# Performance work log

Hardware: AMD Instinct MI355X
Metric: run time of the kernel (lower is better)

Reference implementation:

```python
import jax, jax.numpy as jnp
import numpy as np

DIM = 256
HID = int(DIM * 2.66)        # 680
CH = 2 * HID                 # 1360, TVConv channels
K = 3
K2 = K * K
HP, WP = 14, 14
POSI = 4
INTER = min(64, HID // 2)    # 64
EPS = 1e-5


def conv2d(x, w, pad):
    # x: (B, Cin, H, W), w: (Cout, Cin, kh, kw)
    return jax.lax.conv_general_dilated(
        x, w, window_strides=(1, 1), padding=[(pad, pad), (pad, pad)],
        dimension_numbers=("NCHW", "OIHW", "NCHW"))


def layernorm_chw(x, g, b):
    # torch nn.LayerNorm([C, H, W]): normalize over last 3 dims, affine (C,H,W)
    mu = jnp.mean(x, axis=(1, 2, 3), keepdims=True)
    var = jnp.var(x, axis=(1, 2, 3), keepdims=True)
    return (x - mu) * jax.lax.rsqrt(var + EPS) * g + b


def weight_layers(posi_map, w0, g0, b0, w1, g1, b1, w2, g2, b2, wf):
    h = jax.nn.relu(layernorm_chw(conv2d(posi_map, w0, 1), g0, b0))
    h = jax.nn.relu(layernorm_chw(conv2d(h, w1, 1), g1, b1))
    h = jax.nn.relu(layernorm_chw(conv2d(h, w2, 1), g2, b2))
    return conv2d(h, wf, 1)  # (1, CH*K2, HP, WP)


def tvconv(x, weight):
    # x: (B, CH, HP, WP); weight: (1, CH, K2, HP, WP)
    B, C, H, W = x.shape
    xp = jnp.pad(x, ((0, 0), (0, 0), (1, 1), (1, 1)))
    # unfold ordering: channel-major, kernel positions row-major -> axis=2
    patches = jnp.stack([xp[:, :, i:i + H, j:j + W]
                         for i in range(K) for j in range(K)], axis=2)
    return jnp.sum(weight * patches, axis=2)  # (B, CH, H, W)


def frfn_forward(x, W_in, posi_map, w0, g0, b0, w1, g1, b1, w2, g2, b2, wf, W_out):
    h = jnp.einsum('oc,bchw->bohw', W_in, x)                      # project_in (1x1)
    wgt = weight_layers(posi_map, w0, g0, b0, w1, g1, b1, w2, g2, b2, wf)
    wgt = wgt.reshape(1, CH, K2, HP, WP)
    h = tvconv(h, wgt)                                            # (B, CH, H, W)
    x1, x2 = h[:, :HID], h[:, HID:]
    h = jax.nn.gelu(x1, approximate=False) * x2
    return jnp.einsum('oc,bchw->bohw', W_out, h)                  # project_out (1x1)


def setup_inputs() -> dict:
    key = jax.random.key(0)
    ks = jax.random.split(key, 16)
    s = 0.02
    out_chans = CH * K2
    return {
        "x": jax.random.normal(ks[0], (64, DIM, HP, WP), jnp.float32),
        "W_in": jax.random.normal(ks[1], (CH, DIM), jnp.float32) * s,
        "posi_map": jnp.ones((1, POSI, HP, WP), jnp.float32),
        "w0": jax.random.normal(ks[2], (INTER, POSI, K, K), jnp.float32) * s,
        "g0": jnp.ones((INTER, HP, WP), jnp.float32),
        "b0": jnp.zeros((INTER, HP, WP), jnp.float32),
        "w1": jax.random.normal(ks[3], (INTER, INTER, K, K), jnp.float32) * s,
        "g1": jnp.ones((INTER, HP, WP), jnp.float32),
        "b1": jnp.zeros((INTER, HP, WP), jnp.float32),
        "w2": jax.random.normal(ks[4], (INTER, INTER, K, K), jnp.float32) * s,
        "g2": jnp.ones((INTER, HP, WP), jnp.float32),
        "b2": jnp.zeros((INTER, HP, WP), jnp.float32),
        "wf": jax.random.normal(ks[5], (out_chans, INTER, K, K), jnp.float32) * s,
        "W_out": jax.random.normal(ks[6], (DIM, HID), jnp.float32) * s,
    }


def reference(x, W_in, posi_map, w0, g0, b0, w1, g1, b1, w2, g2, b2, wf, W_out):
    return frfn_forward(x, W_in, posi_map, w0, g0, b0, w1, g1, b1, w2, g2, b2, wf, W_out)
```

## Files before the change

kernel.cpp:

```cpp
#include <hip/hip_runtime.h>
#include <math.h>

#define DIMC   256
#define HID    680
#define CHN    1360
#define HP     14
#define WP     14
#define P      196
#define POSI   4
#define INTER  64
#define BATCH  64
#define KPAD   704
#define OUTCH  12240
#define MW     1408
#define MTOT   12672
#define KIM    576
#define MPADIN 1408
#define EPSLN  1e-5f

typedef __attribute__((ext_vector_type(8))) short short8;
typedef __attribute__((ext_vector_type(4))) short short4v;
typedef __attribute__((ext_vector_type(4))) float f32x4;

#define OFS_WBIN  0u
#define OFS_WBOUT 720896u
#define OFS_XT    1081344u
#define OFS_V0    7503872u
#define OFS_V1    7554048u
#define OFS_V2    7604224u
#define OFS_WGTT  7654656u
#define OFS_H1T   12452736u
#define OFS_HGT   46580608u
#define OFS_IMC   64242560u
#define OFS_WFB   64468352u
#define OFS_PST   79066496u

__device__ __forceinline__ unsigned short f2bf(float f) {
    union { float f; unsigned u; } v; v.f = f;
    unsigned u = v.u;
    return (unsigned short)((u + 0x7FFFu + ((u >> 16) & 1u)) >> 16);
}
__device__ __forceinline__ float bf2f(unsigned short h) {
    union { unsigned u; float f; } v; v.u = ((unsigned)h) << 16; return v.f;
}

__device__ __forceinline__ void gl2lds16(const unsigned short* g, unsigned short* l) {
    __builtin_amdgcn_global_load_lds(
        (const __attribute__((address_space(1))) unsigned int*)g,
        (__attribute__((address_space(3))) unsigned int*)l, 16, 0, 0);
}
__device__ __forceinline__ short8 fragld64(const unsigned short* S, int row, int lp) {
    int slot = ((row >> 1) + lp) & 7;
    return *(const short8*)(S + row * 64 + slot * 8);
}

__device__ __forceinline__ void block_reduce2(float& s, float& ss, float* red, int tid, int nthreads) {
    #pragma unroll
    for (int off = 32; off > 0; off >>= 1) {
        s  += __shfl_down(s, off);
        ss += __shfl_down(ss, off);
    }
    int wid = tid >> 6, nw = nthreads >> 6;
    if ((tid & 63) == 0) { red[wid*2] = s; red[wid*2+1] = ss; }
    __syncthreads();
    if (tid == 0) {
        float S = 0.f, SS = 0.f;
        for (int i = 0; i < nw; i++) { S += red[i*2]; SS += red[i*2+1]; }
        red[0] = S; red[1] = SS;
    }
    __syncthreads();
    s = red[0]; ss = red[1];
}

__device__ __forceinline__ void sum_pstat(const float* __restrict__ pstat, int base,
                                          float& s, float& ss) {
    s = 0.f; ss = 0.f;
    #pragma unroll
    for (int i = 0; i < 49; i++) {
        s  += pstat[base + 2*i];
        ss += pstat[base + 2*i + 1];
    }
}

#define NWIN  (MPADIN*DIMC)
#define NWOUT (DIMC*KPAD)
#define XT0   49
#define WF0   561
#define C0    2343
#define IMZ0  2475
#define PRE_BLKS 2489

__global__ __launch_bounds__(256) void k_pre(const float* __restrict__ Win,
                                             const float* __restrict__ Wout,
                                             const float* __restrict__ x,
                                             const float* __restrict__ wf,
                                             const float* __restrict__ posi,
                                             const float* __restrict__ w0,
                                             unsigned short* __restrict__ Wbin,
                                             unsigned short* __restrict__ Wbout,
                                             unsigned short* __restrict__ Xt,
                                             unsigned short* __restrict__ wfb,
                                             unsigned short* __restrict__ imc,
                                             float* __restrict__ v0,
                                             float* __restrict__ pstat) {
    __shared__ __align__(16) float smem[6304];
    int bid = blockIdx.x, tid = threadIdx.x;
    if (bid < XT0) {
        float (*ppad)[16][16] = (float(*)[16][16])smem;
        float* red = smem + 1024;
        for (int i = tid; i < POSI * 256; i += 256) {
            int cc = i >> 8, r = i & 255, ly = r >> 4, lx = r & 15;
            float v = 0.f;
            if (ly >= 1 && ly <= HP && lx >= 1 && lx <= WP) v = posi[cc*P + (ly-1)*WP + (lx-1)];
            ppad[cc][ly][lx] = v;
        }
        __syncthreads();
        int gid = bid * 256 + tid;
        int c = gid / P, p = gid - c*P, y = p / WP, x2 = p - (p/WP)*WP;
        float v = 0.f;
        #pragma unroll
        for (int ci = 0; ci < POSI; ci++) {
            const float* wr = w0 + (c*POSI + ci)*9;
            v += wr[0]*ppad[ci][y  ][x2] + wr[1]*ppad[ci][y  ][x2+1] + wr[2]*ppad[ci][y  ][x2+2]
               + wr[3]*ppad[ci][y+1][x2] + wr[4]*ppad[ci][y+1][x2+1] + wr[5]*ppad[ci][y+1][x2+2]
               + wr[6]*ppad[ci][y+2][x2] + wr[7]*ppad[ci][y+2][x2+1] + wr[8]*ppad[ci][y+2][x2+2];
        }
        v0[gid] = v;
        float s = v, ss = v * v;
        block_reduce2(s, ss, red, tid, 256);
        if (tid == 0) { pstat[2*bid] = s; pstat[2*bid + 1] = ss; }
    } else if (bid < WF0) {
        int b2 = bid - XT0;
        int b = b2 >> 3, c0 = (b2 & 7) * 32;
        float* xs = smem;
        for (int i = tid; i < 32 * 49; i += 256) {
            int ci = i / 49, p4 = (i - ci * 49) * 4;
            float4 v = *(const float4*)(x + ((size_t)b * DIMC + c0 + ci) * P + p4);
            float* d = xs + ci * 197 + p4;
            d[0] = v.x; d[1] = v.y; d[2] = v.z; d[3] = v.w;
        }
        __syncthreads();
        for (int j = tid; j < P * 4; j += 256) {
            int pp = j >> 2, c8 = (j & 3) * 8;
            short8 o;
            #pragma unroll
            for (int e = 0; e < 8; e++) o[e] = (short)f2bf(xs[(c8 + e) * 197 + pp]);
            *(short8*)(Xt + ((size_t)b * P + pp) * DIMC + c0 + c8) = o;
        }
    } else if (bid < C0) {
        int base = (bid - WF0) * 1024;
        #pragma unroll
        for (int k2 = 0; k2 < 4; k2++) {
            int t = base + k2 * 256 + tid;
            int j = t * 4;
            int rowi = j / KIM, q = j - rowi * KIM;
            int kk = rowi / MW, ch = rowi - kk * MW;
            short4v sv = (short4v)0;
            if (ch < CHN) {
                float4 v = *(const float4*)(wf + ((size_t)(ch * 9 + kk)) * KIM + q);
                sv[0] = (short)f2bf(v.x); sv[1] = (short)f2bf(v.y);
                sv[2] = (short)f2bf(v.z); sv[3] = (short)f2bf(v.w);
            }
            *(short4v*)(wfb + j) = sv;
        }
    } else if (bid < IMZ0) {
        int base = (bid - C0) * 1024;
        #pragma unroll
        for (int k2 = 0; k2 < 4; k2++) {
            int t = base + k2 * 256 + tid;
            int i0 = t * 4;
            if (i0 < NWIN) {
                short4v sv = (short4v)0;
                if (i0 < CHN * DIMC) {
                    float4 v = *(const float4*)(Win + i0);
                    sv[0] = (short)f2bf(v.x); sv[1] = (short)f2bf(v.y);
                    sv[2] = (short)f2bf(v.z); sv[3] = (short)f2bf(v.w);
                }
                *(short4v*)(Wbin + i0) = sv;
            } else {
                int j0 = i0 - NWIN;
                int o = j0 / KPAD, k = j0 - o * KPAD;
                short4v sv = (short4v)0;
                if (k < HID) {
                    float4 v = *(const float4*)(Wout + o * HID + k);
                    sv[0] = (short)f2bf(v.x); sv[1] = (short)f2bf(v.y);
                    sv[2] = (short)f2bf(v.z); sv[3] = (short)f2bf(v.w);
                }
                *(short4v*)(Wbout + j0) = sv;
            }
        }
    } else {
        int base = (bid - IMZ0) * 1024;
        #pragma unroll
        for (int k2 = 0; k2 < 4; k2++) {
            int cc = base + k2 * 256 + tid;
            if (cc < (P * KIM) / 8) *(short8*)(imc + cc * 8) = (short8)0;
        }
    }
}


__device__ __forceinline__ void dev_convln(char* sm, int bid, int tid,
                                           const float* __restrict__ v_in,
                                           const float* __restrict__ g,
                                           const float* __restrict__ b,
                                           const float* __restrict__ w,
                                           float* __restrict__ v_out,
                                           float* __restrict__ pstat,
                                           int psi, int pso) {
    float* asf = (float*)sm;
    float* wlf = asf + INTER * 256;
    float* red = wlf + 3 * INTER * 12;
    const float inv = 1.f / (float)(INTER * P);
    float s0, ss0;
    sum_pstat(pstat, psi, s0, ss0);
    float mu = s0 * inv;
    float var = ss0 * inv - mu * mu;
    float rstd = rsqrtf(var + EPSLN);

    int gid0 = bid * 256;
    int cA = gid0 / P;
    for (int i = tid; i < 3 * INTER * 9; i += 256) {
        int cc = i / (INTER * 9), rest = i - cc * (INTER * 9);
        int ci = rest / 9, kk = rest - ci * 9;
        int crow = cA + cc; if (crow >= INTER) crow = INTER - 1;
        wlf[cc * (INTER * 12) + ci * 12 + kk] = w[(crow * INTER + ci) * 9 + kk];
    }
    for (int i = tid; i < INTER * 64; i += 256)
        *(f32x4*)(asf + i * 4) = (f32x4)0.f;
    __syncthreads();
    #pragma unroll
    for (int it = 0; it < 13; it++) {
        int q4 = it * 256 + tid;
        if (q4 < (INTER * P) / 4) {
            float4 vv = *(const float4*)(v_in + q4 * 4);
            float4 gg = *(const float4*)(g + q4 * 4);
            float4 bb = *(const float4*)(b + q4 * 4);
            float va[4] = {vv.x, vv.y, vv.z, vv.w};
            float ga[4] = {gg.x, gg.y, gg.z, gg.w};
            float ba[4] = {bb.x, bb.y, bb.z, bb.w};
            #pragma unroll
            for (int e = 0; e < 4; e++) {
                int idx = q4 * 4 + e;
                int ci = idx / P, p = idx - ci * P;
                int yy = p / WP, xx = p - yy * WP;
                float a = (va[e] - mu) * rstd * ga[e] + ba[e];
                asf[ci * 256 + (yy + 1) * 16 + (xx + 1)] = a > 0.f ? a : 0.f;
            }
        }
    }
    __syncthreads();
    int gid = gid0 + tid;
    int c = gid / P, p = gid - c * P, y = p / WP, x = p - (p / WP) * WP;
    const float* wr0 = wlf + (c - cA) * (INTER * 12);
    float v = 0.f;
    for (int ci = 0; ci < INTER; ci++) {
        const float* wi = wr0 + ci * 12;
        const float* a0 = asf + ci * 256 + y * 16 + x;
        v += wi[0]*a0[0]  + wi[1]*a0[1]  + wi[2]*a0[2]
           + wi[3]*a0[16] + wi[4]*a0[17] + wi[5]*a0[18]
           + wi[6]*a0[32] + wi[7]*a0[33] + wi[8]*a0[34];
    }
    v_out[gid] = v;
    float s = v, ss = v * v;
    block_reduce2(s, ss, red, tid, 256);
    if (tid == 0) { pstat[pso + 2*bid] = s; pstat[pso + 2*bid + 1] = ss; }
}

__device__ __forceinline__ void dev_lnsc(int bid, int tid,
                                         const float* __restrict__ v_in,
                                         const float* __restrict__ g,
                                         const float* __restrict__ b,
                                         const float* __restrict__ pstat,
                                         unsigned short* __restrict__ imc) {
    const float inv = 1.f / (float)(INTER * P);
    int gid = bid * 256 + tid;
    float s0, ss0;
    sum_pstat(pstat, 196, s0, ss0);
    float mu = s0 * inv;
    float var = ss0 * inv - mu * mu;
    float rstd = rsqrtf(var + EPSLN);
    float a = (v_in[gid] - mu) * rstd * g[gid] + b[gid];
    a = a > 0.f ? a : 0.f;
    unsigned short bv = f2bf(a);
    int ci = gid / P, p = gid - ci * P, y = p / WP, x = p - (p / WP) * WP;
    #pragma unroll
    for (int k = 0; k < 9; k++) {
        int yp = y - (k / 3 - 1), xp = x - (k % 3 - 1);
        if (yp >= 0 && yp < HP && xp >= 0 && xp < WP)
            imc[(yp * WP + xp) * KIM + ci * 9 + k] = bv;
    }
}

#define GIN_MT 11
#define GIN_NT 98
#define GIN_BLKS (GIN_MT * GIN_NT)
__device__ __forceinline__ void dev_gemm_in(char* sm, int mb, int nb, int tid,
                                            const unsigned short* __restrict__ A,
                                            const unsigned short* __restrict__ B,
                                            unsigned short* __restrict__ C) {
    unsigned short* As = (unsigned short*)sm;
    unsigned short* Bs = As + 128 * 64;
    int w = tid >> 6, lane = tid & 63, quad = lane >> 4, c16 = lane & 15;
    int m0 = mb * 128, n0 = nb * 128;
    int wm = (w & 1) * 64, wn = (w >> 1) * 64;
    f32x4 acc[4][4];
    #pragma unroll
    for (int i = 0; i < 4; i++)
        #pragma unroll
        for (int j = 0; j < 4; j++) acc[i][j] = (f32x4)0.f;

    for (int kc = 0; kc < 4; ++kc) {
        int k0 = kc * 64;
        if (kc) __syncthreads();
        #pragma unroll
        for (int i = tid; i < 1024; i += 256) {
            int r = i >> 3, s = i & 7, q = (s - (r >> 1)) & 7;
            gl2lds16(A + (size_t)(m0 + r) * DIMC + k0 + q * 8, As + (i & ~63) * 8);
        }
        #pragma unroll
        for (int i = tid; i < 1024; i += 256) {
            int r = i >> 3, s = i & 7, q = (s - (r >> 1)) & 7;
            gl2lds16(B + (size_t)(n0 + r) * DIMC + k0 + q * 8, Bs + (i & ~63) * 8);
        }
        __syncthreads();
        #pragma unroll
        for (int ks = 0; ks < 2; ++ks) {
            short8 af[4], bfr[4];
            #pragma unroll
            for (int i = 0; i < 4; i++) af[i] = fragld64(As, wm + i * 16 + c16, ks * 4 + quad);
            #pragma unroll
            for (int j = 0; j < 4; j++) bfr[j] = fragld64(Bs, wn + j * 16 + c16, ks * 4 + quad);
            #pragma unroll
            for (int i = 0; i < 4; i++)
                #pragma unroll
                for (int j = 0; j < 4; j++)
                    acc[i][j] = __builtin_amdgcn_mfma_f32_16x16x32_bf16(af[i], bfr[j], acc[i][j], 0, 0, 0);
        }
    }
    #pragma unroll
    for (int j = 0; j < 4; j++) {
        int n = n0 + wn + j * 16 + c16;
        unsigned short* dst = C + (size_t)n * CHN;
        #pragma unroll
        for (int i = 0; i < 4; i++) {
            int m = m0 + wm + i * 16 + quad * 4;
            if (m < CHN) {
                short4v sv;
                sv[0] = (short)f2bf(acc[i][j][0]);
                sv[1] = (short)f2bf(acc[i][j][1]);
                sv[2] = (short)f2bf(acc[i][j][2]);
                sv[3] = (short)f2bf(acc[i][j][3]);
                *(short4v*)(dst + m) = sv;
            }
        }
    }
}

__device__ __forceinline__ void dev_gemm_wf(char* sm, int bid, int tid,
                                            const unsigned short* __restrict__ wfb,
                                            const unsigned short* __restrict__ imc,
                                            unsigned short* __restrict__ wgtT) {
    unsigned short* buf = (unsigned short*)sm;
    unsigned short* As = buf;
    unsigned short* Bs = buf + 64 * 64;
    unsigned short* ot = buf;
    int w = tid >> 6, lane = tid & 63, quad = lane >> 4, c16 = lane & 15;
    int m0 = bid * 64;
    int kk = m0 / MW, ch0 = m0 - kk * MW;
    for (int i = tid; i < 96; i += 256)
        *(short8*)(Bs + 196 * 64 + i * 8) = (short8)0;
    f32x4 acc[13];
    #pragma unroll
    for (int f = 0; f < 13; f++) acc[f] = (f32x4)0.f;

    for (int kc = 0; kc < 9; ++kc) {
        int k0 = kc * 64;
        if (kc) __syncthreads();
        #pragma unroll
        for (int i = tid; i < 512; i += 256) {
            int r = i >> 3, s = i & 7, q = (s - (r >> 1)) & 7;
            gl2lds16(wfb + ((size_t)(kk * MW + ch0 + r)) * KIM + k0 + q * 8, As + (i & ~63) * 8);
        }
        for (int i = tid; i < 1568; i += 256) {
            int r = i >> 3, s = i & 7, q = (s - (r >> 1)) & 7;
            gl2lds16(imc + (size_t)r * KIM + k0 + q * 8, Bs + (i & ~63) * 8);
        }
        __syncthreads();
        #pragma unroll
        for (int ks = 0; ks < 2; ++ks) {
            short8 af = fragld64(As, w * 16 + c16, ks * 4 + quad);
            #pragma unroll
            for (int f = 0; f < 13; f++) {
                short8 bf = fragld64(Bs, f * 16 + c16, ks * 4 + quad);
                acc[f] = __builtin_amdgcn_mfma_f32_16x16x32_bf16(af, bf, acc[f], 0, 0, 0);
            }
        }
    }
    __syncthreads();
    #pragma unroll
    for (int f = 0; f < 13; f++) {
        int p = f * 16 + c16;
        if (p < P) {
            short4v sv;
            sv[0] = (short)f2bf(acc[f][0]);
            sv[1] = (short)f2bf(acc[f][1]);
            sv[2] = (short)f2bf(acc[f][2]);
            sv[3] = (short)f2bf(acc[f][3]);
            *(short4v*)(ot + p * 72 + w * 16 + quad * 4) = sv;
        }
    }
    __syncthreads();
    int nvalid = CHN - ch0; if (nvalid > 64) nvalid = 64;
    for (int p = tid; p < P; p += 256) {
        const short8* src = (const short8*)(ot + p * 72);
        unsigned short* dst = wgtT + ((size_t)p * 9 + kk) * CHN + ch0;
        #pragma unroll
        for (int j = 0; j < 8; j++)
            if (j * 8 < nvalid) *(short8*)(dst + j * 8) = src[j];
    }
}

#define SLICE 210
#define CONVLN_LDS ((INTER*256 + 3*INTER*12 + 16) * 4)
#define GEMMWF_LDS ((64*64 + 208*64) * 2)

extern __shared__ char dynsm[];

__global__ __launch_bounds__(256) void k_mA(const float* v0, const float* g0,
                                            const float* b0, const float* w1,
                                            float* v1, float* pstat,
                                            const unsigned short* Wbin,
                                            const unsigned short* Xt,
                                            unsigned short* h1t) {
    int bid = blockIdx.x, tid = threadIdx.x;
    if (bid < 49) dev_convln(dynsm, bid, tid, v0, g0, b0, w1, v1, pstat, 0, 98);
    else { int fid = bid - 49; dev_gemm_in(dynsm, fid % GIN_MT, fid / GIN_MT, tid, Wbin, Xt, h1t); }
}
__global__ __launch_bounds__(256) void k_mB(const float* v1, const float* g1,
                                            const float* b1, const float* w2,
                                            float* v2, float* pstat,
                                            const unsigned short* Wbin,
                                            const unsigned short* Xt,
                                            unsigned short* h1t) {
    int bid = blockIdx.x, tid = threadIdx.x;
    if (bid < 49) dev_convln(dynsm, bid, tid, v1, g1, b1, w2, v2, pstat, 98, 196);
    else { int fid = SLICE + bid - 49; dev_gemm_in(dynsm, fid % GIN_MT, fid / GIN_MT, tid, Wbin, Xt, h1t); }
}
__global__ __launch_bounds__(256) void k_mC(const float* v2, const float* g2,
                                            const float* b2, const float* pstat,
                                            unsigned short* imc,
                                            const unsigned short* Wbin,
                                            const unsigned short* Xt,
                                            unsigned short* h1t) {
    int bid = blockIdx.x, tid = threadIdx.x;
    if (bid < 49) dev_lnsc(bid, tid, v2, g2, b2, pstat, imc);
    else { int fid = 2 * SLICE + bid - 49; dev_gemm_in(dynsm, fid % GIN_MT, fid / GIN_MT, tid, Wbin, Xt, h1t); }
}
__global__ __launch_bounds__(256) void k_mD(const unsigned short* wfb,
                                            const unsigned short* imc,
                                            unsigned short* wgtT,
                                            const unsigned short* Wbin,
                                            const unsigned short* Xt,
                                            unsigned short* h1t) {
    int bid = blockIdx.x, tid = threadIdx.x;
    if (bid < 198) dev_gemm_wf(dynsm, bid, tid, wfb, imc, wgtT);
    else { int fid = 3 * SLICE + bid - 198; dev_gemm_in(dynsm, fid % GIN_MT, fid / GIN_MT, tid, Wbin, Xt, h1t); }
}

__global__ __launch_bounds__(256) void k_tvg(const unsigned short* __restrict__ h1t,
                                             const unsigned short* __restrict__ wgtT,
                                             unsigned short* __restrict__ hgt) {
    __shared__ __align__(16) unsigned short wl[9 * CHN];
    int id = blockIdx.x;
    int xcd = id & 7, q = id >> 3;
    int p = xcd * 25 + (q % 25);
    int bg = q / 25;
    if (p >= P) return;
    int b0 = bg * 8, tid = threadIdx.x;
    const unsigned short* wrow = wgtT + (size_t)p * 9 * CHN;
    for (int i = tid * 8; i < 9 * CHN; i += 256 * 8)
        *(short8*)(wl + i) = *(const short8*)(wrow + i);
    int y = p / WP, x = p - (p / WP) * WP;
    int pn[9]; bool pv[9];
    #pragma unroll
    for (int k = 0; k < 9; k++) {
        int yy = y + k / 3 - 1, xx = x + (k % 3) - 1;
        pv[k] = (yy >= 0 && yy < HP && xx >= 0 && xx < WP);
        pn[k] = pv[k] ? yy * WP + xx : 0;
    }
    __syncthreads();
    for (int j = tid; j < 8 * 85; j += 256) {
        int bl = j / 85, c = (j - bl * 85) * 8;
        int b = b0 + bl;
        const unsigned short* hb = h1t + (size_t)b * P * CHN;
        float s1[8], s2[8];
        #pragma unroll
        for (int e = 0; e < 8; e++) { s1[e] = 0.f; s2[e] = 0.f; }
        #pragma unroll
        for (int k = 0; k < 9; k++) {
            if (!pv[k]) continue;
            const unsigned short* hr = hb + (size_t)pn[k] * CHN + c;
            short8 h1v = *(const short8*)hr;
            short8 h2v = *(const short8*)(hr + HID);
            short8 w1v = *(const short8*)(wl + k * CHN + c);
            short8 w2v = *(const short8*)(wl + k * CHN + HID + c);
            #pragma unroll
            for (int e = 0; e < 8; e++) {
                s1[e] += bf2f((unsigned short)w1v[e]) * bf2f((unsigned short)h1v[e]);
                s2[e] += bf2f((unsigned short)w2v[e]) * bf2f((unsigned short)h2v[e]);
            }
        }
        short8 o;
        #pragma unroll
        for (int e = 0; e < 8; e++) {
            float gl = 0.5f * s1[e] * (1.f + erff(s1[e] * 0.70710678118654752f));
            o[e] = (short)f2bf(gl * s2[e]);
        }
        *(short8*)(hgt + ((size_t)b * P + p) * KPAD + c) = o;
    }
    if (tid < 24) {
        int bl = tid / 3, z = (tid - bl * 3) * 8;
        *(short8*)(hgt + ((size_t)(b0 + bl) * P + p) * KPAD + HID + z) = (short8)0;
    }
}

__global__ __launch_bounds__(256) void k_gemm_out(const unsigned short* __restrict__ A,
                                                  const unsigned short* __restrict__ B,
                                                  float* __restrict__ out) {
    __shared__ __align__(16) unsigned short As[64 * 64];
    __shared__ __align__(16) unsigned short Bs[128 * 64];
    int tid = threadIdx.x;
    int w = tid >> 6, lane = tid & 63, quad = lane >> 4, c16 = lane & 15;
    int m0 = blockIdx.x * 64, n0 = blockIdx.y * 128;
    int wm = (w & 1) * 32, wn = (w >> 1) * 64;
    f32x4 acc[2][4];
    #pragma unroll
    for (int i = 0; i < 2; i++)
        #pragma unroll
        for (int j = 0; j < 4; j++) acc[i][j] = (f32x4)0.f;

    for (int kc = 0; kc < 11; ++kc) {
        int k0 = kc * 64;
        if (kc) __syncthreads();
        #pragma unroll
        for (int i = tid; i < 512; i += 256) {
            int r = i >> 3, s = i & 7, q = (s - (r >> 1)) & 7;
            gl2lds16(A + (size_t)(m0 + r) * KPAD + k0 + q * 8, As + (i & ~63) * 8);
        }
        #pragma unroll
        for (int i = tid; i < 1024; i += 256) {
            int r = i >> 3, s = i & 7, q = (s - (r >> 1)) & 7;
            gl2lds16(B + (size_t)(n0 + r) * KPAD + k0 + q * 8, Bs + (i & ~63) * 8);
        }
        __syncthreads();
        #pragma unroll
        for (int ks = 0; ks < 2; ++ks) {
            short8 af[2], bfr[4];
            #pragma unroll
            for (int i = 0; i < 2; i++) af[i] = fragld64(As, wm + i * 16 + c16, ks * 4 + quad);
            #pragma unroll
            for (int j = 0; j < 4; j++) bfr[j] = fragld64(Bs, wn + j * 16 + c16, ks * 4 + quad);
            #pragma unroll
            for (int i = 0; i < 2; i++)
                #pragma unroll
                for (int j = 0; j < 4; j++)
                    acc[i][j] = __builtin_amdgcn_mfma_f32_16x16x32_bf16(af[i], bfr[j], acc[i][j], 0, 0, 0);
        }
    }
    #pragma unroll
    for (int j = 0; j < 4; j++) {
        int n = n0 + wn + j * 16 + c16;
        int b = n / P, pp = n - b * P;
        #pragma unroll
        for (int i = 0; i < 2; i++) {
            int m = m0 + wm + i * 16 + quad * 4;
            #pragma unroll
            for (int r = 0; r < 4; r++)
                out[((size_t)b * DIMC + m + r) * P + pp] = acc[i][j][r];
        }
    }
}

extern "C" void kernel_launch(void* const* d_in, const int* in_sizes, int n_in,
                              void* d_out, int out_size, void* d_ws, size_t ws_size,
                              hipStream_t stream) {
    (void)in_sizes; (void)n_in; (void)out_size; (void)ws_size;
    const float* x     = (const float*)d_in[0];
    const float* W_in  = (const float*)d_in[1];
    const float* posi  = (const float*)d_in[2];
    const float* w0    = (const float*)d_in[3];
    const float* g0    = (const float*)d_in[4];
    const float* b0    = (const float*)d_in[5];
    const float* w1    = (const float*)d_in[6];
    const float* g1    = (const float*)d_in[7];
    const float* b1    = (const float*)d_in[8];
    const float* w2    = (const float*)d_in[9];
    const float* g2    = (const float*)d_in[10];
    const float* b2    = (const float*)d_in[11];
    const float* wf    = (const float*)d_in[12];
    const float* W_out = (const float*)d_in[13];
    float* out = (float*)d_out;
    char* ws = (char*)d_ws;

    unsigned short* Wbin  = (unsigned short*)(ws + OFS_WBIN);
    unsigned short* Wbout = (unsigned short*)(ws + OFS_WBOUT);
    unsigned short* Xt    = (unsigned short*)(ws + OFS_XT);
    float*          v0    = (float*)(ws + OFS_V0);
    float*          v1    = (float*)(ws + OFS_V1);
    float*          v2    = (float*)(ws + OFS_V2);
    float*          pstat = (float*)(ws + OFS_PST);
    unsigned short* wgtT  = (unsigned short*)(ws + OFS_WGTT);
    unsigned short* h1t   = (unsigned short*)(ws + OFS_H1T);
    unsigned short* hgt   = (unsigned short*)(ws + OFS_HGT);
    unsigned short* imc   = (unsigned short*)(ws + OFS_IMC);
    unsigned short* wfb   = (unsigned short*)(ws + OFS_WFB);

    k_pre<<<PRE_BLKS, 256, 0, stream>>>(
        W_in, W_out, x, wf, posi, w0, Wbin, Wbout, Xt, wfb, imc, v0, pstat);
    k_mA<<<49 + SLICE, 256, CONVLN_LDS, stream>>>(v0, g0, b0, w1, v1, pstat, Wbin, Xt, h1t);
    k_mB<<<49 + SLICE, 256, CONVLN_LDS, stream>>>(v1, g1, b1, w2, v2, pstat, Wbin, Xt, h1t);
    k_mC<<<49 + SLICE, 256, CONVLN_LDS, stream>>>(v2, g2, b2, pstat, imc, Wbin, Xt, h1t);
    k_mD<<<198 + (GIN_BLKS - 3 * SLICE), 256, GEMMWF_LDS, stream>>>(wfb, imc, wgtT, Wbin, Xt, h1t);
    k_tvg     <<<1600, 256, 0, stream>>>(h1t, wgtT, hgt);
    k_gemm_out<<<dim3(DIMC/64, (BATCH*P)/128), 256, 0, stream>>>(Wbout, hgt, out);
}
```

Measured before the change: 217.9 us.

## Move fused stage kernels to 512 threads and widen project-in GEMM tile to 128x256

The four fused stage kernels now launch 512-thread blocks. The project-in GEMM tile widens from 128x128 to 128x256, so each A tile is reused across twice as many columns and the block count halves. The wf GEMM splits its 13 column fragments across two groups of four waves, and the conv/LN helpers stride by 512 with only the first 256 threads doing the conv. The per-kernel GEMM slice boundaries are rebalanced to match. This cuts redundant A loads and block overhead, but larger blocks with a large LDS allocation may reduce occupancy, and threads 256–511 sit idle in the conv and LN parts.

```diff
diff --git a/kernel.cpp b/kernel.cpp
--- a/kernel.cpp
+++ b/kernel.cpp
@@ -220,18 +220,18 @@
 
     int gid0 = bid * 256;
     int cA = gid0 / P;
-    for (int i = tid; i < 3 * INTER * 9; i += 256) {
+    for (int i = tid; i < 3 * INTER * 9; i += 512) {
         int cc = i / (INTER * 9), rest = i - cc * (INTER * 9);
         int ci = rest / 9, kk = rest - ci * 9;
         int crow = cA + cc; if (crow >= INTER) crow = INTER - 1;
         wlf[cc * (INTER * 12) + ci * 12 + kk] = w[(crow * INTER + ci) * 9 + kk];
     }
-    for (int i = tid; i < INTER * 64; i += 256)
+    for (int i = tid; i < INTER * 64; i += 512)
         *(f32x4*)(asf + i * 4) = (f32x4)0.f;
     __syncthreads();
     #pragma unroll
-    for (int it = 0; it < 13; it++) {
-        int q4 = it * 256 + tid;
+    for (int it = 0; it < 7; it++) {
+        int q4 = it * 512 + tid;
         if (q4 < (INTER * P) / 4) {
             float4 vv = *(const float4*)(v_in + q4 * 4);
             float4 gg = *(const float4*)(g + q4 * 4);
@@ -250,20 +250,23 @@
         }
     }
     __syncthreads();
-    int gid = gid0 + tid;
-    int c = gid / P, p = gid - c * P, y = p / WP, x = p - (p / WP) * WP;
-    const float* wr0 = wlf + (c - cA) * (INTER * 12);
-    float v = 0.f;
-    for (int ci = 0; ci < INTER; ci++) {
-        const float* wi = wr0 + ci * 12;
-        const float* a0 = asf + ci * 256 + y * 16 + x;
-        v += wi[0]*a0[0]  + wi[1]*a0[1]  + wi[2]*a0[2]
-           + wi[3]*a0[16] + wi[4]*a0[17] + wi[5]*a0[18]
-           + wi[6]*a0[32] + wi[7]*a0[33] + wi[8]*a0[34];
-    }
-    v_out[gid] = v;
-    float s = v, ss = v * v;
-    block_reduce2(s, ss, red, tid, 256);
+    float s = 0.f, ss = 0.f;
+    if (tid < 256) {
+        int gid = gid0 + tid;
+        int c = gid / P, p = gid - c * P, y = p / WP, x = p - (p / WP) * WP;
+        const float* wr0 = wlf + (c - cA) * (INTER * 12);
+        float v = 0.f;
+        for (int ci = 0; ci < INTER; ci++) {
+            const float* wi = wr0 + ci * 12;
+            const float* a0 = asf + ci * 256 + y * 16 + x;
+            v += wi[0]*a0[0]  + wi[1]*a0[1]  + wi[2]*a0[2]
+               + wi[3]*a0[16] + wi[4]*a0[17] + wi[5]*a0[18]
+               + wi[6]*a0[32] + wi[7]*a0[33] + wi[8]*a0[34];
+        }
+        v_out[gid] = v;
+        s = v; ss = v * v;
+    }
+    block_reduce2(s, ss, red, tid, 512);
     if (tid == 0) { pstat[pso + 2*bid] = s; pstat[pso + 2*bid + 1] = ss; }
 }
 
@@ -273,6 +276,7 @@
                                          const float* __restrict__ b,
                                          const float* __restrict__ pstat,
                                          unsigned short* __restrict__ imc) {
+    if (tid >= 256) return;
     const float inv = 1.f / (float)(INTER * P);
     int gid = bid * 256 + tid;
     float s0, ss0;
@@ -293,7 +297,7 @@
 }
 
 #define GIN_MT 11
-#define GIN_NT 98
+#define GIN_NT 49
 #define GIN_BLKS (GIN_MT * GIN_NT)
 __device__ __forceinline__ void dev_gemm_in(char* sm, int mb, int nb, int tid,
                                             const unsigned short* __restrict__ A,
@@ -302,7 +306,7 @@
     unsigned short* As = (unsigned short*)sm;
     unsigned short* Bs = As + 128 * 64;
     int w = tid >> 6, lane = tid & 63, quad = lane >> 4, c16 = lane & 15;
-    int m0 = mb * 128, n0 = nb * 128;
+    int m0 = mb * 128, n0 = nb * 256;
     int wm = (w & 1) * 64, wn = (w >> 1) * 64;
     f32x4 acc[4][4];
     #pragma unroll
@@ -314,12 +318,12 @@
         int k0 = kc * 64;
         if (kc) __syncthreads();
         #pragma unroll
-        for (int i = tid; i < 1024; i += 256) {
+        for (int i = tid; i < 1024; i += 512) {
             int r = i >> 3, s = i & 7, q = (s - (r >> 1)) & 7;
             gl2lds16(A + (size_t)(m0 + r) * DIMC + k0 + q * 8, As + (i & ~63) * 8);
         }
         #pragma unroll
-        for (int i = tid; i < 1024; i += 256) {
+        for (int i = tid; i < 2048; i += 512) {
             int r = i >> 3, s = i & 7, q = (s - (r >> 1)) & 7;
             gl2lds16(B + (size_t)(n0 + r) * DIMC + k0 + q * 8, Bs + (i & ~63) * 8);
         }
@@ -366,53 +370,60 @@
     unsigned short* Bs = buf + 64 * 64;
     unsigned short* ot = buf;
     int w = tid >> 6, lane = tid & 63, quad = lane >> 4, c16 = lane & 15;
+    int wq = w & 3;
+    int f0 = (w < 4) ? 0 : 7;
+    int fN = (w < 4) ? 7 : 6;
     int m0 = bid * 64;
     int kk = m0 / MW, ch0 = m0 - kk * MW;
-    for (int i = tid; i < 96; i += 256)
+    for (int i = tid; i < 96; i += 512)
         *(short8*)(Bs + 196 * 64 + i * 8) = (short8)0;
-    f32x4 acc[13];
-    #pragma unroll
-    for (int f = 0; f < 13; f++) acc[f] = (f32x4)0.f;
+    f32x4 acc[7];
+    #pragma unroll
+    for (int f = 0; f < 7; f++) acc[f] = (f32x4)0.f;
 
     for (int kc = 0; kc < 9; ++kc) {
         int k0 = kc * 64;
         if (kc) __syncthreads();
-        #pragma unroll
-        for (int i = tid; i < 512; i += 256) {
+        {
+            int i = tid;
             int r = i >> 3, s = i & 7, q = (s - (r >> 1)) & 7;
             gl2lds16(wfb + ((size_t)(kk * MW + ch0 + r)) * KIM + k0 + q * 8, As + (i & ~63) * 8);
         }
-        for (int i = tid; i < 1568; i += 256) {
+        for (int i = tid; i < 1568; i += 512) {
             int r = i >> 3, s = i & 7, q = (s - (r >> 1)) & 7;
             gl2lds16(imc + (size_t)r * KIM + k0 + q * 8, Bs + (i & ~63) * 8);
         }
         __syncthreads();
         #pragma unroll
         for (int ks = 0; ks < 2; ++ks) {
-            short8 af = fragld64(As, w * 16 + c16, ks * 4 + quad);
-            #pragma unroll
-            for (int f = 0; f < 13; f++) {
-                short8 bf = fragld64(Bs, f * 16 + c16, ks * 4 + quad);
-                acc[f] = __builtin_amdgcn_mfma_f32_16x16x32_bf16(af, bf, acc[f], 0, 0, 0);
+            short8 af = fragld64(As, wq * 16 + c16, ks * 4 + quad);
+            #pragma unroll
+            for (int f = 0; f < 7; f++) {
+                if (f < fN) {
+                    short8 bf = fragld64(Bs, (f0 + f) * 16 + c16, ks * 4 + quad);
+                    acc[f] = __builtin_amdgcn_mfma_f32_16x16x32_bf16(af, bf, acc[f], 0, 0, 0);
+                }
             }
         }
     }
     __syncthreads();
     #pragma unroll
-    for (int f = 0; f < 13; f++) {
-        int p = f * 16 + c16;
-        if (p < P) {
-            short4v sv;
-            sv[0] = (short)f2bf(acc[f][0]);
-            sv[1] = (short)f2bf(acc[f][1]);
-            sv[2] = (short)f2bf(acc[f][2]);
-            sv[3] = (short)f2bf(acc[f][3]);
-            *(short4v*)(ot + p * 72 + w * 16 + quad * 4) = sv;
+    for (int f = 0; f < 7; f++) {
+        if (f < fN) {
+            int p = (f0 + f) * 16 + c16;
+            if (p < P) {
+                short4v sv;
+                sv[0] = (short)f2bf(acc[f][0]);
+                sv[1] = (short)f2bf(acc[f][1]);
+                sv[2] = (short)f2bf(acc[f][2]);
+                sv[3] = (short)f2bf(acc[f][3]);
+                *(short4v*)(ot + p * 72 + wq * 16 + quad * 4) = sv;
+            }
         }
     }
     __syncthreads();
     int nvalid = CHN - ch0; if (nvalid > 64) nvalid = 64;
-    for (int p = tid; p < P; p += 256) {
+    for (int p = tid; p < P; p += 512) {
         const short8* src = (const short8*)(ot + p * 72);
         unsigned short* dst = wgtT + ((size_t)p * 9 + kk) * CHN + ch0;
         #pragma unroll
@@ -421,13 +432,16 @@
     }
 }
 
-#define SLICE 210
+#define FA 0
+#define FB 161
+#define FC 321
+#define FD 481
 #define CONVLN_LDS ((INTER*256 + 3*INTER*12 + 16) * 4)
-#define GEMMWF_LDS ((64*64 + 208*64) * 2)
+#define GIN_LDS    ((128*64 + 256*64) * 2)
 
 extern __shared__ char dynsm[];
 
-__global__ __launch_bounds__(256) void k_mA(const float* v0, const float* g0,
+__global__ __launch_bounds__(512) void k_mA(const float* v0, const float* g0,
                                             const float* b0, const float* w1,
                                             float* v1, float* pstat,
                                             const unsigned short* Wbin,
@@ -435,9 +449,9 @@
                                             unsigned short* h1t) {
     int bid = blockIdx.x, tid = threadIdx.x;
     if (bid < 49) dev_convln(dynsm, bid, tid, v0, g0, b0, w1, v1, pstat, 0, 98);
-    else { int fid = bid - 49; dev_gemm_in(dynsm, fid % GIN_MT, fid / GIN_MT, tid, Wbin, Xt, h1t); }
-}
-__global__ __launch_bounds__(256) void k_mB(const float* v1, const float* g1,
+    else { int fid = FA + bid - 49; dev_gemm_in(dynsm, fid % GIN_MT, fid / GIN_MT, tid, Wbin, Xt, h1t); }
+}
+__global__ __launch_bounds__(512) void k_mB(const float* v1, const float* g1,
                                             const float* b1, const float* w2,
                                             float* v2, float* pstat,
                                             const unsigned short* Wbin,
@@ -445,9 +459,9 @@
                                             unsigned short* h1t) {
     int bid = blockIdx.x, tid = threadIdx.x;
     if (bid < 49) dev_convln(dynsm, bid, tid, v1, g1, b1, w2, v2, pstat, 98, 196);
-    else { int fid = SLICE + bid - 49; dev_gemm_in(dynsm, fid % GIN_MT, fid / GIN_MT, tid, Wbin, Xt, h1t); }
-}
-__global__ __launch_bounds__(256) void k_mC(const float* v2, const float* g2,
+    else { int fid = FB + bid - 49; dev_gemm_in(dynsm, fid % GIN_MT, fid / GIN_MT, tid, Wbin, Xt, h1t); }
+}
+__global__ __launch_bounds__(512) void k_mC(const float* v2, const float* g2,
                                             const float* b2, const float* pstat,
                                             unsigned short* imc,
                                             const unsigned short* Wbin,
@@ -455,9 +469,9 @@
                                             unsigned short* h1t) {
     int bid = blockIdx.x, tid = threadIdx.x;
     if (bid < 49) dev_lnsc(bid, tid, v2, g2, b2, pstat, imc);
-    else { int fid = 2 * SLICE + bid - 49; dev_gemm_in(dynsm, fid % GIN_MT, fid / GIN_MT, tid, Wbin, Xt, h1t); }
-}
-__global__ __launch_bounds__(256) void k_mD(const unsigned short* wfb,
+    else { int fid = FC + bid - 49; dev_gemm_in(dynsm, fid % GIN_MT, fid / GIN_MT, tid, Wbin, Xt, h1t); }
+}
+__global__ __launch_bounds__(512) void k_mD(const unsigned short* wfb,
                                             const unsigned short* imc,
                                             unsigned short* wgtT,
                                             const unsigned short* Wbin,
@@ -465,7 +479,7 @@
                                             unsigned short* h1t) {
     int bid = blockIdx.x, tid = threadIdx.x;
     if (bid < 198) dev_gemm_wf(dynsm, bid, tid, wfb, imc, wgtT);
-    else { int fid = 3 * SLICE + bid - 198; dev_gemm_in(dynsm, fid % GIN_MT, fid / GIN_MT, tid, Wbin, Xt, h1t); }
+    else { int fid = FD + bid - 198; dev_gemm_in(dynsm, fid % GIN_MT, fid / GIN_MT, tid, Wbin, Xt, h1t); }
 }
 
 __global__ __launch_bounds__(256) void k_tvg(const unsigned short* __restrict__ h1t,
@@ -618,10 +632,10 @@
 
     k_pre<<<PRE_BLKS, 256, 0, stream>>>(
         W_in, W_out, x, wf, posi, w0, Wbin, Wbout, Xt, wfb, imc, v0, pstat);
-    k_mA<<<49 + SLICE, 256, CONVLN_LDS, stream>>>(v0, g0, b0, w1, v1, pstat, Wbin, Xt, h1t);
-    k_mB<<<49 + SLICE, 256, CONVLN_LDS, stream>>>(v1, g1, b1, w2, v2, pstat, Wbin, Xt, h1t);
-    k_mC<<<49 + SLICE, 256, CONVLN_LDS, stream>>>(v2, g2, b2, pstat, imc, Wbin, Xt, h1t);
-    k_mD<<<198 + (GIN_BLKS - 3 * SLICE), 256, GEMMWF_LDS, stream>>>(wfb, imc, wgtT, Wbin, Xt, h1t);
+    k_mA<<<49 + (FB - FA), 512, CONVLN_LDS, stream>>>(v0, g0, b0, w1, v1, pstat, Wbin, Xt, h1t);
+    k_mB<<<49 + (FC - FB), 512, CONVLN_LDS, stream>>>(v1, g1, b1, w2, v2, pstat, Wbin, Xt, h1t);
+    k_mC<<<49 + (FD - FC), 512, CONVLN_LDS, stream>>>(v2, g2, b2, pstat, imc, Wbin, Xt, h1t);
+    k_mD<<<198 + (GIN_BLKS - FD), 512, GIN_LDS, stream>>>(wfb, imc, wgtT, Wbin, Xt, h1t);
     k_tvg     <<<1600, 256, 0, stream>>>(h1t, wgtT, hgt);
     k_gemm_out<<<dim3(DIMC/64, (BATCH*P)/128), 256, 0, stream>>>(Wbout, hgt, out);
 }
```

Result: faster. 212.8 us (-2.3%).
